# Optimization experiments

Hardware: AMD Instinct MI355X
Metric: run time of the kernel (lower is better)

## Reference

```python
import jax, jax.numpy as jnp
import numpy as np


def _nn_sq_dists(query, ref):
    # query: [B, N, 3], ref: [B, M, 3]
    # squared distance via ||q||^2 + ||r||^2 - 2 q.r, min over ref points
    q2 = jnp.sum(query * query, axis=-1)            # [B, N]
    r2 = jnp.sum(ref * ref, axis=-1)                # [B, M]
    cross = jnp.einsum('bnc,bmc->bnm', query, ref)  # [B, N, M]
    d = q2[:, :, None] + r2[:, None, :] - 2.0 * cross
    d = jnp.maximum(d, 0.0)  # clamp numerical negatives (true distances >= 0)
    return jnp.min(d, axis=-1)                      # [B, N] 1-NN squared dists


def setup_inputs() -> dict:
    key = jax.random.key(0)
    k1, k2 = jax.random.split(key)
    B, C, N = 4, 3, 8192
    pc2 = jax.random.normal(k1, (B, C, N), dtype=jnp.float32)
    pc1_warped = jax.random.normal(k2, (B, C, N), dtype=jnp.float32)
    return {"pc2": pc2, "pc1_warped": pc1_warped}


def reference(pc2, pc1_warped):
    # pos1 = target['pc2'], pos2 = output['pc1_warped'], both [B, 3, N]
    pos1 = jnp.transpose(pc2, (0, 2, 1))         # [B, N, 3]
    pos2 = jnp.transpose(pc1_warped, (0, 2, 1))  # [B, N, 3]
    # pointutils.knn(1, pos1, pos2): for each pos1 point, nearest in pos2.
    nn_d = _nn_sq_dists(pos1, pos2)              # [B, N]
    per_batch = jnp.sum(nn_d, axis=1)            # sum over dim 1
    loss = per_batch.mean() + per_batch.mean()
    return loss
```

## Files before the change

kernel.cpp:

```cpp
#include <hip/hip_runtime.h>


#define NPTS 8192
#define NB   4
#define RR   8
#define WPB  8
#define BT   (WPB * 64)

typedef float f32x16 __attribute__((ext_vector_type(16)));
typedef short bf16x8 __attribute__((ext_vector_type(8)));

static __device__ __forceinline__ unsigned int f2bf(float f) {
    unsigned int u = __float_as_uint(f);
    u += 0x7FFF + ((u >> 16) & 1);
    return u >> 16;
}
static __device__ __forceinline__ float bf2f(unsigned int s) {
    return __uint_as_float(s << 16);
}

__global__ __launch_bounds__(512) void chamfer_prep(
    const float* __restrict__ pc1w,
    uint4* __restrict__ wsA,
    float* __restrict__ out)
{
    const int g = blockIdx.x * 512 + threadIdx.x;
    if (g == 0) out[0] = 0.0f;
    const int b = g >> 13, i = g & (NPTS - 1);
    const float* refb = pc1w + b * 3 * NPTS;
    float x = refb[i], y = refb[NPTS + i], z = refb[2 * NPTS + i];
    unsigned xh = f2bf(x), yh = f2bf(y), zh = f2bf(z);
    unsigned xl = f2bf(x - bf2f(xh));
    unsigned yl = f2bf(y - bf2f(yh));
    unsigned zl = f2bf(z - bf2f(zh));
    float h = -0.5f * (x * x + y * y + z * z);
    unsigned hh = f2bf(h);
    unsigned hl = f2bf(h - bf2f(hh));
    const int rr = i >> 10, ir = i & 1023, c = ir >> 5, l = ir & 31;
    uint4* dst = wsA + (((b * RR + rr) * 32 + c) << 6);
    dst[l]      = make_uint4(xh | (xl << 16), xh | (yh << 16),
                             yl | (yh << 16), zh | (zl << 16));
    dst[32 + l] = make_uint4(zh | (hh << 16), hl, 0u, 0u);
}

static __device__ __forceinline__ void stage_range(
    const uint4* __restrict__ gsrc, uint4* lbase, int wave, int lane)
{
#pragma unroll
    for (int j = 0; j < 4; ++j) {
        const int idx = j * 512 + wave * 64;
        const uint4* gp = gsrc + idx + lane;
        uint4* lp = lbase + idx;
        __builtin_amdgcn_global_load_lds(
            (const __attribute__((address_space(1))) unsigned int*)gp,
            (__attribute__((address_space(3))) unsigned int*)lp, 16, 0, 0);
    }
}

static __device__ __forceinline__ bf16x8 make_bfrag(float x, float y, float z,
                                                    int lane)
{
    unsigned xh = f2bf(x), yh = f2bf(y), zh = f2bf(z);
    unsigned xl = f2bf(x - bf2f(xh));
    unsigned yl = f2bf(y - bf2f(yh));
    unsigned zl = f2bf(z - bf2f(zh));
    uint4 bu = (lane < 32)
        ? make_uint4(xh | (xh << 16), xl | (yh << 16),
                     yh | (yl << 16), zh | (zh << 16))
        : make_uint4(zl | (0x3F80u << 16), 0x3F80u, 0u, 0u);
    return __builtin_bit_cast(bf16x8, bu);
}

static __device__ __forceinline__ void proc_chunk(
    uint4 av, bf16x8 bq0, bf16x8 bq1, const f32x16& zero,
    float& rma0, float& rma1, float& rma2, float& rma3,
    float& rmb0, float& rmb1, float& rmb2, float& rmb3)
{
    bf16x8 aa = __builtin_bit_cast(bf16x8, av);
    f32x16 d0 = __builtin_amdgcn_mfma_f32_32x32x16_bf16(aa, bq0, zero, 0, 0, 0);
    f32x16 d1 = __builtin_amdgcn_mfma_f32_32x32x16_bf16(aa, bq1, zero, 0, 0, 0);
    rma0 = fmaxf(rma0, fmaxf(d0[0],  d0[1]));
    rma0 = fmaxf(rma0, fmaxf(d0[2],  d0[3]));
    rma1 = fmaxf(rma1, fmaxf(d0[4],  d0[5]));
    rma1 = fmaxf(rma1, fmaxf(d0[6],  d0[7]));
    rma2 = fmaxf(rma2, fmaxf(d0[8],  d0[9]));
    rma2 = fmaxf(rma2, fmaxf(d0[10], d0[11]));
    rma3 = fmaxf(rma3, fmaxf(d0[12], d0[13]));
    rma3 = fmaxf(rma3, fmaxf(d0[14], d0[15]));
    rmb0 = fmaxf(rmb0, fmaxf(d1[0],  d1[1]));
    rmb0 = fmaxf(rmb0, fmaxf(d1[2],  d1[3]));
    rmb1 = fmaxf(rmb1, fmaxf(d1[4],  d1[5]));
    rmb1 = fmaxf(rmb1, fmaxf(d1[6],  d1[7]));
    rmb2 = fmaxf(rmb2, fmaxf(d1[8],  d1[9]));
    rmb2 = fmaxf(rmb2, fmaxf(d1[10], d1[11]));
    rmb3 = fmaxf(rmb3, fmaxf(d1[12], d1[13]));
    rmb3 = fmaxf(rmb3, fmaxf(d1[14], d1[15]));
}

__global__ __launch_bounds__(BT, 4) void chamfer_main(
    const float* __restrict__ pc2,
    const uint4* __restrict__ wsA,
    float* __restrict__ out)
{
    __shared__ uint4 abuf[2][2048];
    __shared__ float red[WPB][64];
    const int tid  = threadIdx.x;
    const int wave = tid >> 6;
    const int lane = tid & 63;
    const int b    = blockIdx.y;
    const int qc0  = blockIdx.x * 2;

    const float* qb = pc2 + b * 3 * NPTS;
    const int qn0 = qc0 * 32 + (lane & 31);
    const int qn1 = qn0 + 32;
    float x0 = qb[qn0], y0 = qb[NPTS + qn0], z0 = qb[2 * NPTS + qn0];
    float x1 = qb[qn1], y1 = qb[NPTS + qn1], z1 = qb[2 * NPTS + qn1];

    const uint4* wsb = wsA + (size_t)b * RR * 2048;
    stage_range(wsb, abuf[0], wave, lane);

    bf16x8 bq0 = make_bfrag(x0, y0, z0, lane);
    bf16x8 bq1 = make_bfrag(x1, y1, z1, lane);

    f32x16 zero;
#pragma unroll
    for (int i = 0; i < 16; ++i) zero[i] = 0.0f;

    float rma0 = -3e38f, rma1 = -3e38f, rma2 = -3e38f, rma3 = -3e38f;
    float rmb0 = -3e38f, rmb1 = -3e38f, rmb2 = -3e38f, rmb3 = -3e38f;

#pragma unroll
    for (int p = 0; p < RR; ++p) {
        if (p != RR - 1) {
            stage_range(wsb + (p + 1) * 2048, abuf[(p + 1) & 1], wave, lane);
            asm volatile("s_waitcnt vmcnt(4)" ::: "memory");
        } else {
            asm volatile("s_waitcnt vmcnt(0)" ::: "memory");
        }
        __builtin_amdgcn_s_barrier();
        asm volatile("" ::: "memory");

        const uint4* src = &abuf[p & 1][wave * 256];
        uint4 av0 = src[lane];
        uint4 av1 = src[64 + lane];
        uint4 av2 = src[128 + lane];
        uint4 av3 = src[192 + lane];
        proc_chunk(av0, bq0, bq1, zero, rma0, rma1, rma2, rma3,
                   rmb0, rmb1, rmb2, rmb3);
        proc_chunk(av1, bq0, bq1, zero, rma0, rma1, rma2, rma3,
                   rmb0, rmb1, rmb2, rmb3);
        proc_chunk(av2, bq0, bq1, zero, rma0, rma1, rma2, rma3,
                   rmb0, rmb1, rmb2, rmb3);
        proc_chunk(av3, bq0, bq1, zero, rma0, rma1, rma2, rma3,
                   rmb0, rmb1, rmb2, rmb3);

        if (p != RR - 1) {
            asm volatile("" ::: "memory");
            __builtin_amdgcn_s_barrier();
        }
    }

    float rma = fmaxf(fmaxf(rma0, rma1), fmaxf(rma2, rma3));
    float rmb = fmaxf(fmaxf(rmb0, rmb1), fmaxf(rmb2, rmb3));
    rma = fmaxf(rma, __shfl_xor(rma, 32, 64));
    rmb = fmaxf(rmb, __shfl_xor(rmb, 32, 64));
    if (lane < 32) {
        red[wave][lane]      = rma;
        red[wave][32 + lane] = rmb;
    }
    __syncthreads();

    if (tid < 64) {
        float smax = red[0][tid];
#pragma unroll
        for (int w = 1; w < WPB; ++w) smax = fmaxf(smax, red[w][tid]);
        const int n = qc0 * 32 + tid;
        float qx = qb[n], qy = qb[NPTS + n], qz = qb[2 * NPTS + n];
        float d = fmaxf(qx * qx + qy * qy + qz * qz - 2.0f * smax, 0.0f);
#pragma unroll
        for (int off = 32; off > 0; off >>= 1)
            d += __shfl_down(d, off, 64);
        if (tid == 0)
            atomicAdd(out, d * (2.0f / NB));
    }
}

extern "C" void kernel_launch(void* const* d_in, const int* in_sizes, int n_in,
                              void* d_out, int out_size, void* d_ws, size_t ws_size,
                              hipStream_t stream) {
    const float* pc2  = (const float*)d_in[0];
    const float* pc1w = (const float*)d_in[1];
    float* out = (float*)d_out;
    uint4* wsA = (uint4*)d_ws;

    chamfer_prep<<<NB * NPTS / 512, 512, 0, stream>>>(pc1w, wsA, out);
    dim3 g(128, NB);
    chamfer_main<<<g, BT, 0, stream>>>(pc2, wsA, out);
}
```

Measured before the change: 79.79 us.

## Replace LDS double-buffered staging with direct per-wave global loads

Drops the shared-memory double buffer and the global_load_lds staging with its block-wide barriers. Each wave now reads its own contiguous slice of 32 reference chunks straight from global memory, with a one-deep register prefetch. The prep layout becomes a flat per-batch chunk array so each wave's slice is contiguous. This removes barrier synchronisation and LDS traffic, but relies on L2/cache for reuse across blocks and gives a shallower latency-hiding prefetch.

```diff
diff --git a/kernel.cpp b/kernel.cpp
--- a/kernel.cpp
+++ b/kernel.cpp
@@ -3,9 +3,9 @@
 
 #define NPTS 8192
 #define NB   4
-#define RR   8
 #define WPB  8
 #define BT   (WPB * 64)
+#define CPW  32
 
 typedef float f32x16 __attribute__((ext_vector_type(16)));
 typedef short bf16x8 __attribute__((ext_vector_type(8)));
@@ -36,25 +36,11 @@
     float h = -0.5f * (x * x + y * y + z * z);
     unsigned hh = f2bf(h);
     unsigned hl = f2bf(h - bf2f(hh));
-    const int rr = i >> 10, ir = i & 1023, c = ir >> 5, l = ir & 31;
-    uint4* dst = wsA + (((b * RR + rr) * 32 + c) << 6);
+    const int c = i >> 5, l = i & 31;
+    uint4* dst = wsA + (((size_t)b * 256 + c) << 6);
     dst[l]      = make_uint4(xh | (xl << 16), xh | (yh << 16),
                              yl | (yh << 16), zh | (zl << 16));
     dst[32 + l] = make_uint4(zh | (hh << 16), hl, 0u, 0u);
-}
-
-static __device__ __forceinline__ void stage_range(
-    const uint4* __restrict__ gsrc, uint4* lbase, int wave, int lane)
-{
-#pragma unroll
-    for (int j = 0; j < 4; ++j) {
-        const int idx = j * 512 + wave * 64;
-        const uint4* gp = gsrc + idx + lane;
-        uint4* lp = lbase + idx;
-        __builtin_amdgcn_global_load_lds(
-            (const __attribute__((address_space(1))) unsigned int*)gp,
-            (__attribute__((address_space(3))) unsigned int*)lp, 16, 0, 0);
-    }
 }
 
 static __device__ __forceinline__ bf16x8 make_bfrag(float x, float y, float z,
@@ -102,7 +88,6 @@
     const uint4* __restrict__ wsA,
     float* __restrict__ out)
 {
-    __shared__ uint4 abuf[2][2048];
     __shared__ float red[WPB][64];
     const int tid  = threadIdx.x;
     const int wave = tid >> 6;
@@ -115,10 +100,6 @@
     const int qn1 = qn0 + 32;
     float x0 = qb[qn0], y0 = qb[NPTS + qn0], z0 = qb[2 * NPTS + qn0];
     float x1 = qb[qn1], y1 = qb[NPTS + qn1], z1 = qb[2 * NPTS + qn1];
-
-    const uint4* wsb = wsA + (size_t)b * RR * 2048;
-    stage_range(wsb, abuf[0], wave, lane);
-
     bf16x8 bq0 = make_bfrag(x0, y0, z0, lane);
     bf16x8 bq1 = make_bfrag(x1, y1, z1, lane);
 
@@ -129,35 +110,16 @@
     float rma0 = -3e38f, rma1 = -3e38f, rma2 = -3e38f, rma3 = -3e38f;
     float rmb0 = -3e38f, rmb1 = -3e38f, rmb2 = -3e38f, rmb3 = -3e38f;
 
-#pragma unroll
-    for (int p = 0; p < RR; ++p) {
-        if (p != RR - 1) {
-            stage_range(wsb + (p + 1) * 2048, abuf[(p + 1) & 1], wave, lane);
-            asm volatile("s_waitcnt vmcnt(4)" ::: "memory");
-        } else {
-            asm volatile("s_waitcnt vmcnt(0)" ::: "memory");
-        }
-        __builtin_amdgcn_s_barrier();
-        asm volatile("" ::: "memory");
+    const uint4* src = wsA + (((size_t)b * 256 + wave * CPW) << 6);
 
-        const uint4* src = &abuf[p & 1][wave * 256];
-        uint4 av0 = src[lane];
-        uint4 av1 = src[64 + lane];
-        uint4 av2 = src[128 + lane];
-        uint4 av3 = src[192 + lane];
-        proc_chunk(av0, bq0, bq1, zero, rma0, rma1, rma2, rma3,
+    uint4 av = src[lane];
+#pragma unroll 4
+    for (int c = 0; c < CPW; ++c) {
+        uint4 acur = av;
+        if (c + 1 < CPW)
+            av = src[((c + 1) << 6) + lane];
+        proc_chunk(acur, bq0, bq1, zero, rma0, rma1, rma2, rma3,
                    rmb0, rmb1, rmb2, rmb3);
-        proc_chunk(av1, bq0, bq1, zero, rma0, rma1, rma2, rma3,
-                   rmb0, rmb1, rmb2, rmb3);
-        proc_chunk(av2, bq0, bq1, zero, rma0, rma1, rma2, rma3,
-                   rmb0, rmb1, rmb2, rmb3);
-        proc_chunk(av3, bq0, bq1, zero, rma0, rma1, rma2, rma3,
-                   rmb0, rmb1, rmb2, rmb3);
-
-        if (p != RR - 1) {
-            asm volatile("" ::: "memory");
-            __builtin_amdgcn_s_barrier();
-        }
     }
 
     float rma = fmaxf(fmaxf(rma0, rma1), fmaxf(rma2, rma3));
```

After: 76.06 us. 4.7% less time.
